# Kernel optimization log

Measured on AMD Instinct MI355X. Metric: run time of the kernel, lower is better.

## Reference

```python
import jax, jax.numpy as jnp
import numpy as np

L, B, S, H, NH, F = 4, 2, 1024, 1024, 16, 4096
DH = H // NH

def setup_inputs() -> dict:
    key = jax.random.key(0)
    ks = jax.random.split(key, 16)
    std = 0.02
    return {
        'x': jax.random.normal(ks[0], (B, S, H), jnp.float32),
        'attention_mask': jnp.ones((B, S, S), jnp.float32),
        'wq': jax.random.normal(ks[1], (L, H, H), jnp.float32) * std,
        'bq': jnp.zeros((L, H), jnp.float32),
        'wk': jax.random.normal(ks[2], (L, H, H), jnp.float32) * std,
        'bk': jnp.zeros((L, H), jnp.float32),
        'wv': jax.random.normal(ks[3], (L, H, H), jnp.float32) * std,
        'bv': jnp.zeros((L, H), jnp.float32),
        'wo_attn': jax.random.normal(ks[4], (L, H, H), jnp.float32) * std,
        'bo_attn': jnp.zeros((L, H), jnp.float32),
        'alpha_attn': jax.random.uniform(ks[5], (L,), jnp.float32) * 0.1,
        'wi': jax.random.normal(ks[6], (L, H, F), jnp.float32) * std,
        'bi': jnp.zeros((L, F), jnp.float32),
        'wo_ffn': jax.random.normal(ks[7], (L, F, H), jnp.float32) * std,
        'bo_ffn': jnp.zeros((L, H), jnp.float32),
        'alpha_ffn': jax.random.uniform(ks[8], (L,), jnp.float32) * 0.1,
    }

def _heads(t):
    # [B,S,H] -> [B,NH,S,DH]
    return t.reshape(B, S, NH, DH).transpose(0, 2, 1, 3)

def reference(x, attention_mask, wq, bq, wk, bk, wv, bv, wo_attn, bo_attn,
              alpha_attn, wi, bi, wo_ffn, bo_ffn, alpha_ffn):
    # additive mask: (1 - mask) * -10000, broadcast over heads
    adder = (1.0 - attention_mask)[:, None, :, :] * -10000.0  # [B,1,S,S]
    scale = 1.0 / jnp.sqrt(jnp.asarray(DH, x.dtype))
    for l in range(L):
        q = _heads(x @ wq[l] + bq[l])
        k = _heads(x @ wk[l] + bk[l])
        v = _heads(x @ wv[l] + bv[l])
        scores = jnp.einsum('bhqd,bhkd->bhqk', q, k) * scale + adder
        probs = jax.nn.softmax(scores, axis=-1)
        ctx = jnp.einsum('bhqk,bhkd->bhqd', probs, v)
        ctx = ctx.transpose(0, 2, 1, 3).reshape(B, S, H)
        attn_out = ctx @ wo_attn[l] + bo_attn[l]
        x = x + alpha_attn[l] * attn_out  # rezero residual
        inter = jax.nn.gelu(x @ wi[l] + bi[l], approximate=True)
        ffn_out = inter @ wo_ffn[l] + bo_ffn[l]
        x = x + alpha_ffn[l] * ffn_out  # rezero residual
    return x
```

## Files before the change

kernel.cpp:

```cpp
#include <hip/hip_runtime.h>
#include <cstdint>

#define B_  2
#define S_  1024
#define H_  1024
#define NH_ 16
#define DH_ 64
#define F_  4096
#define L_  4
#define M_  (B_*S_)

typedef __bf16 bf16;
typedef __bf16 bf16x8 __attribute__((ext_vector_type(8)));
typedef __bf16 bf16x4 __attribute__((ext_vector_type(4)));
typedef __bf16 bf16x2 __attribute__((ext_vector_type(2)));
typedef float  f32x4  __attribute__((ext_vector_type(4)));

__device__ __forceinline__ void async_ld16(void* lds, const void* g) {
  auto* lp = reinterpret_cast<__attribute__((address_space(3))) unsigned int*>(
      reinterpret_cast<uintptr_t>(lds));
  const auto* gp = reinterpret_cast<const __attribute__((address_space(1))) unsigned int*>(
      reinterpret_cast<uintptr_t>(g));
  __builtin_amdgcn_global_load_lds(gp, lp, 16, 0, 0);
}

__device__ __forceinline__ float gelu_tanh(float x) {
  float u = 0.7978845608028654f * (x + 0.044715f * x * x * x);
  u = fminf(fmaxf(u, -15.f), 15.f);
  float e = __builtin_amdgcn_exp2f(u * 2.8853900817779268f);
  return 0.5f * x * (1.f + (e - 1.f) / (e + 1.f));
}

__global__ __launch_bounds__(256) void transpose_all(
    const float* __restrict__ wq, const float* __restrict__ wk,
    const float* __restrict__ wv, const float* __restrict__ wo,
    const float* __restrict__ wi, const float* __restrict__ wf,
    bf16* __restrict__ WtQKV, bf16* __restrict__ WtO,
    bf16* __restrict__ WtI, bf16* __restrict__ WtF) {
  const size_t HH = (size_t)H_ * H_;
  const size_t HF = (size_t)H_ * F_;
  int idx = blockIdx.x;
  const float* src;
  bf16* dst;
  int N, K, k0, n0;
  if (idx < 4096) {
    const int s = idx >> 10;
    const int l = (idx >> 8) & 3;
    const int t = idx & 255;
    n0 = (t & 15) * 64; k0 = (t >> 4) * 64;
    N = H_; K = H_;
    src = (s == 0 ? wq : s == 1 ? wk : s == 2 ? wv : wo) + (size_t)l * HH;
    dst = (s < 3) ? (WtQKV + (size_t)l * 3 * HH + (size_t)s * HH)
                  : (WtO + (size_t)l * HH);
  } else if (idx < 8192) {
    const int j = idx - 4096;
    const int l = j >> 10;
    const int t = j & 1023;
    n0 = (t & 63) * 64; k0 = (t >> 6) * 64;
    N = F_; K = H_;
    src = wi + (size_t)l * HF;
    dst = WtI + (size_t)l * HF;
  } else {
    const int j = idx - 8192;
    const int l = j >> 10;
    const int t = j & 1023;
    n0 = (t & 15) * 64; k0 = (t >> 4) * 64;
    N = H_; K = F_;
    src = wf + (size_t)l * HF;
    dst = WtF + (size_t)l * HF;
  }
  __shared__ float t[64][65];
  const int x = threadIdx.x, y = threadIdx.y;
  #pragma unroll
  for (int i = 0; i < 64; i += 8) {
    const float2 v = *(const float2*)(src + (size_t)(k0 + y + i) * N + n0 + 2 * x);
    t[2 * x][y + i] = v.x;
    t[2 * x + 1][y + i] = v.y;
  }
  __syncthreads();
  #pragma unroll
  for (int i = 0; i < 64; i += 8) {
    bf16x2 o;
    o[0] = (bf16)t[y + i][2 * x];
    o[1] = (bf16)t[y + i][2 * x + 1];
    *(bf16x2*)(dst + (size_t)(n0 + y + i) * K + k0 + 2 * x) = o;
  }
}

__global__ __launch_bounds__(256) void prep_kernel(
    const float4* __restrict__ mask, bf16x4* __restrict__ madd,
    const float4* __restrict__ x, float4* __restrict__ xf,
    bf16x4* __restrict__ xb) {
  const int blk = blockIdx.x;
  if (blk < 2048) {
    const int i = blk * 256 + (int)threadIdx.x;
    const float c2 = -10000.f * 1.44269504088896f;
    float4 v = mask[i];
    bf16x4 o;
    o[0] = (bf16)((1.f - v.x) * c2);
    o[1] = (bf16)((1.f - v.y) * c2);
    o[2] = (bf16)((1.f - v.z) * c2);
    o[3] = (bf16)((1.f - v.w) * c2);
    madd[i] = o;
  } else {
    const int i = (blk - 2048) * 256 + (int)threadIdx.x;
    float4 v = x[i];
    xf[i] = v;
    bf16x4 b;
    b[0] = (bf16)v.x; b[1] = (bf16)v.y; b[2] = (bf16)v.z; b[3] = (bf16)v.w;
    xb[i] = b;
  }
}

__device__ __forceinline__ void gemm_core(
    const bf16* __restrict__ A, const bf16* __restrict__ Bt, int ld, int kLen,
    int m0, int n0, bf16* As, bf16* Bs, f32x4 (&acc)[4][4]) {
  const int tid = (int)threadIdx.x;
  const int w = tid >> 6, l = tid & 63;
  const int lr = l & 15, lg = l >> 4;
  const int wm = w >> 1, wn = w & 1;
  const int srow = l >> 2;
  const int scol = (l & 3) * 8;

  const bf16* ag = A  + (size_t)(m0 + w * 32 + srow) * ld + scol;
  const bf16* bg = Bt + (size_t)(n0 + w * 32 + srow) * ld + scol;
  const int soff = (w * 32) * 32;

  auto stage = [&](int buf, int kk) {
    bf16* ad = As + buf * 4096 + soff;
    bf16* bd = Bs + buf * 4096 + soff;
    async_ld16(ad,           ag + kk);
    async_ld16(ad + 16 * 32, ag + kk + (size_t)16 * ld);
    async_ld16(bd,           bg + kk);
    async_ld16(bd + 16 * 32, bg + kk + (size_t)16 * ld);
  };

  stage(0, 0);
  __syncthreads();
  int cur = 0;
  for (int k0 = 0; k0 < kLen; k0 += 32) {
    if (k0 + 32 < kLen) stage(cur ^ 1, k0 + 32);
    const bf16* Ab = As + cur * 4096;
    const bf16* Bb = Bs + cur * 4096;
    bf16x8 af[4], bv[4];
    #pragma unroll
    for (int i = 0; i < 4; ++i)
      af[i] = *(const bf16x8*)(Ab + (wm * 64 + i * 16 + lr) * 32 + lg * 8);
    #pragma unroll
    for (int i = 0; i < 4; ++i)
      bv[i] = *(const bf16x8*)(Bb + (wn * 64 + i * 16 + lr) * 32 + lg * 8);
    #pragma unroll
    for (int i = 0; i < 4; ++i)
      #pragma unroll
      for (int j = 0; j < 4; ++j)
        acc[i][j] = __builtin_amdgcn_mfma_f32_16x16x32_bf16(af[i], bv[j], acc[i][j], 0, 0, 0);
    __syncthreads();
    cur ^= 1;
  }
}

template <int MODE>
__global__ __launch_bounds__(256) void gemm128_kernel(
    const bf16* __restrict__ A, const bf16* __restrict__ Bt,
    const float* __restrict__ bias, bf16* __restrict__ outb,
    int N, int K, int kSlice) {
  __shared__ __align__(16) bf16 As[2 * 128 * 32];
  __shared__ __align__(16) bf16 Bs[2 * 128 * 32];
  const int m0 = blockIdx.y * 128, n0 = blockIdx.x * 128;
  const int z = blockIdx.z;
  const f32x4 z4 = {0.f, 0.f, 0.f, 0.f};
  f32x4 acc[4][4];
  #pragma unroll
  for (int i = 0; i < 4; ++i)
    #pragma unroll
    for (int j = 0; j < 4; ++j) acc[i][j] = z4;

  gemm_core(A + (size_t)z * kSlice, Bt + (size_t)z * kSlice, K, kSlice,
            m0, n0, As, Bs, acc);

  const int tid = (int)threadIdx.x;
  const int w = tid >> 6, l = tid & 63;
  const int lr = l & 15, lg = l >> 4;
  const int wm = w >> 1, wn = w & 1;
  const size_t pbase = (MODE == 3) ? (size_t)z * M_ * (size_t)N : 0;
  #pragma unroll
  for (int i = 0; i < 4; ++i) {
    const int row0 = m0 + wm * 64 + i * 16 + lg * 4;
    #pragma unroll
    for (int j = 0; j < 4; ++j) {
      const int col = n0 + wn * 64 + j * 16 + lr;
      const float bvx = (MODE == 3) ? 0.f : bias[col];
      #pragma unroll
      for (int r = 0; r < 4; ++r) {
        const size_t idx = (size_t)(row0 + r) * N + col;
        float v = acc[i][j][r] + bvx;
        if (MODE == 3) {
          outb[pbase + idx] = (bf16)v;
        } else {
          outb[idx] = (bf16)gelu_tanh(v);
        }
      }
    }
  }
}

__global__ __launch_bounds__(256) void reduce_residual(
    const bf16x4* __restrict__ part, const float* __restrict__ bias,
    const float* __restrict__ alphap, float4* __restrict__ xf,
    bf16x4* __restrict__ xb) {
  const int i = blockIdx.x * 256 + (int)threadIdx.x;
  const int nper = M_ * H_ / 4;
  float s[4] = {0.f, 0.f, 0.f, 0.f};
  #pragma unroll
  for (int zz = 0; zz < 4; ++zz) {
    const bf16x4 p = part[i + (size_t)zz * nper];
    #pragma unroll
    for (int k = 0; k < 4; ++k) s[k] += (float)p[k];
  }
  const int col = (i * 4) & (H_ - 1);
  const float4 b4 = *(const float4*)(bias + col);
  const float a = *alphap;
  float4 xv = xf[i];
  xv.x += a * (s[0] + b4.x);
  xv.y += a * (s[1] + b4.y);
  xv.z += a * (s[2] + b4.z);
  xv.w += a * (s[3] + b4.w);
  xf[i] = xv;
  bf16x4 bb;
  bb[0] = (bf16)xv.x; bb[1] = (bf16)xv.y; bb[2] = (bf16)xv.z; bb[3] = (bf16)xv.w;
  xb[i] = bb;
}

__global__ __launch_bounds__(256) void gemm_qkv64(
    const bf16* __restrict__ A, const bf16* __restrict__ Wt,
    const float* __restrict__ bq, const float* __restrict__ bk,
    const float* __restrict__ bvv,
    bf16* __restrict__ qo, bf16* __restrict__ ko, bf16* __restrict__ vt) {
  __shared__ __align__(16) bf16 As[2 * 128 * 32];
  __shared__ __align__(16) bf16 Bs[2 * 64 * 32];
  const int tid = (int)threadIdx.x;
  const int w = tid >> 6, l = tid & 63;
  const int lr = l & 15, lg = l >> 4;
  const int wm = w >> 1, wn = w & 1;
  const int srow = l >> 2, scol = (l & 3) * 8;
  const int m0 = blockIdx.y * 128, n0 = blockIdx.x * 64;

  const bf16* ag = A  + (size_t)(m0 + w * 32 + srow) * H_ + scol;
  const bf16* bg = Wt + (size_t)(n0 + w * 16 + srow) * H_ + scol;
  const int aoff = (w * 32) * 32;
  const int boff = (w * 16) * 32;

  auto stage = [&](int buf, int kk) {
    bf16* ad = As + buf * 4096 + aoff;
    bf16* bd = Bs + buf * 2048 + boff;
    async_ld16(ad,           ag + kk);
    async_ld16(ad + 16 * 32, ag + kk + (size_t)16 * H_);
    async_ld16(bd,           bg + kk);
  };

  const f32x4 z4 = {0.f, 0.f, 0.f, 0.f};
  f32x4 acc[4][2];
  #pragma unroll
  for (int i = 0; i < 4; ++i)
    #pragma unroll
    for (int j = 0; j < 2; ++j) acc[i][j] = z4;

  stage(0, 0);
  __syncthreads();
  int cur = 0;
  for (int k0 = 0; k0 < H_; k0 += 32) {
    if (k0 + 32 < H_) stage(cur ^ 1, k0 + 32);
    const bf16* Ab = As + cur * 4096;
    const bf16* Bb = Bs + cur * 2048;
    bf16x8 af[4], bv[2];
    #pragma unroll
    for (int i = 0; i < 4; ++i)
      af[i] = *(const bf16x8*)(Ab + (wm * 64 + i * 16 + lr) * 32 + lg * 8);
    #pragma unroll
    for (int j = 0; j < 2; ++j)
      bv[j] = *(const bf16x8*)(Bb + (wn * 32 + j * 16 + lr) * 32 + lg * 8);
    #pragma unroll
    for (int i = 0; i < 4; ++i)
      #pragma unroll
      for (int j = 0; j < 2; ++j)
        acc[i][j] = __builtin_amdgcn_mfma_f32_16x16x32_bf16(af[i], bv[j], acc[i][j], 0, 0, 0);
    __syncthreads();
    cur ^= 1;
  }

  if (n0 < 2048) {
    bf16* out = (n0 < 1024) ? qo : ko;
    const float* bias = (n0 < 1024) ? bq : bk;
    const int nl = n0 & 1023;
    #pragma unroll
    for (int i = 0; i < 4; ++i) {
      const int row0 = m0 + wm * 64 + i * 16 + lg * 4;
      #pragma unroll
      for (int j = 0; j < 2; ++j) {
        const int col = nl + wn * 32 + j * 16 + lr;
        const float bvx = bias[col];
        #pragma unroll
        for (int r = 0; r < 4; ++r)
          out[(size_t)(row0 + r) * H_ + col] = (bf16)(acc[i][j][r] + bvx);
      }
    }
  } else {
    const int hh = (n0 >> 6) - 32;
    #pragma unroll
    for (int i = 0; i < 4; ++i) {
      const int row0 = m0 + wm * 64 + i * 16 + lg * 4;
      const int bb = row0 >> 10, ss = row0 & (S_ - 1);
      #pragma unroll
      for (int j = 0; j < 2; ++j) {
        const int dd = wn * 32 + j * 16 + lr;
        const float bvx = bvv[hh * 64 + dd];
        bf16x4 pk;
        #pragma unroll
        for (int r = 0; r < 4; ++r) pk[r] = (bf16)(acc[i][j][r] + bvx);
        *(bf16x4*)(vt + (((size_t)(bb * NH_ + hh) * DH_ + dd) << 10) + ss) = pk;
      }
    }
  }
}

__global__ __launch_bounds__(256) void attn_kernel7(
    const bf16* __restrict__ Q, const bf16* __restrict__ Kb,
    const bf16* __restrict__ Vt, const bf16* __restrict__ madd,
    bf16* __restrict__ Ctx) {
  const int tid = (int)threadIdx.x;
  const int w = tid >> 6, l = tid & 63;
  const int lr = l & 15, lg = l >> 4;
  const int r7 = lr & 7;
  const int h = blockIdx.y, b = blockIdx.z;
  const int q0 = blockIdx.x * 64 + w * 16;

  __shared__ __align__(16) bf16 Kt[2][64 * 64];
  __shared__ __align__(16) bf16 Vs[2][64 * 64];
  __shared__ unsigned int Pu[4][16][36];

  const bf16* qp = Q + ((size_t)(b * S_ + q0 + lr)) * H_ + h * DH_;
  const bf16x8 qa0 = *(const bf16x8*)(qp + lg * 8);
  const bf16x8 qa1 = *(const bf16x8*)(qp + 32 + lg * 8);

  const f32x4 z4 = {0.f, 0.f, 0.f, 0.f};
  f32x4 acc[4];
  #pragma unroll
  for (int dt = 0; dt < 4; ++dt) acc[dt] = z4;
  float mrow = -1e30f, ssum = 0.f;

  const bf16* Kbase = Kb + ((size_t)b * S_) * H_ + h * DH_;
  const bf16* Vbase = Vt + ((size_t)(b * NH_ + h)) * DH_ * S_;
  const bf16* Mb = madd + ((size_t)(b * S_ + q0 + lr)) * S_;

  const float c1 = 0.125f * 1.44269504088896f;
  const float THR = 10.f;

  const int sub = l >> 3;
  const int cs  = ((l & 7) ^ sub) * 8;
  auto stage = [&](int buf, int kv) {
    #pragma unroll
    for (int j = 0; j < 2; ++j) {
      const int rbase = w * 16 + j * 8;
      async_ld16(&Kt[buf][rbase * 64],
                 Kbase + (size_t)(kv + rbase + sub) * H_ + cs);
      async_ld16(&Vs[buf][rbase * 64],
                 Vbase + (size_t)(rbase + sub) * S_ + kv + cs);
    }
  };

  stage(0, 0);
  bf16x4 mk[4];
  #pragma unroll
  for (int t = 0; t < 4; ++t) mk[t] = *(const bf16x4*)(Mb + t * 16 + lg * 4);
  __syncthreads();
  int cur = 0;
  #pragma unroll 1
  for (int it = 0; it < 16; ++it) {
    const int kv0 = it * 64;
    if (it < 15) stage(cur ^ 1, kv0 + 64);
    bf16x4 mkn[4];
    if (it < 15) {
      #pragma unroll
      for (int t = 0; t < 4; ++t)
        mkn[t] = *(const bf16x4*)(Mb + kv0 + 64 + t * 16 + lg * 4);
    }
    const bf16* Kc = &Kt[cur][0];
    const bf16* Vc = &Vs[cur][0];
    bf16x8 kf0[4], kf1[4];
    #pragma unroll
    for (int t = 0; t < 4; ++t) {
      kf0[t] = *(const bf16x8*)(Kc + (t * 16 + lr) * 64 + ((lg ^ r7) * 8));
      kf1[t] = *(const bf16x8*)(Kc + (t * 16 + lr) * 64 + (((4 + lg) ^ r7) * 8));
    }
    f32x4 st[4];
    __builtin_amdgcn_s_setprio(1);
    #pragma unroll
    for (int t = 0; t < 4; ++t) {
      f32x4 s = __builtin_amdgcn_mfma_f32_16x16x32_bf16(kf0[t], qa0, z4, 0, 0, 0);
      st[t] = __builtin_amdgcn_mfma_f32_16x16x32_bf16(kf1[t], qa1, s, 0, 0, 0);
    }
    __builtin_amdgcn_s_setprio(0);
    float sv[4][4];
    #pragma unroll
    for (int t = 0; t < 4; ++t)
      #pragma unroll
      for (int r = 0; r < 4; ++r)
        sv[t][r] = st[t][r] * c1 + (float)mk[t][r];
    float nm = sv[0][0];
    #pragma unroll
    for (int t = 0; t < 4; ++t)
      #pragma unroll
      for (int r = 0; r < 4; ++r) nm = fmaxf(nm, sv[t][r]);
    nm = fmaxf(nm, __shfl_xor(nm, 16));
    nm = fmaxf(nm, __shfl_xor(nm, 32));
    if (__any(nm > mrow + THR)) {
      float newm = fmaxf(mrow, nm);
      float f = __builtin_amdgcn_exp2f(mrow - newm);
      mrow = newm;
      ssum *= f;
      #pragma unroll
      for (int dt = 0; dt < 4; ++dt)
        #pragma unroll
        for (int r = 0; r < 4; ++r) acc[dt][r] *= f;
    }
    float p[4][4];
    float ps = 0.f;
    #pragma unroll
    for (int t = 0; t < 4; ++t)
      #pragma unroll
      for (int r = 0; r < 4; ++r) {
        p[t][r] = __builtin_amdgcn_exp2f(sv[t][r] - mrow);
        ps += p[t][r];
      }
    ps += __shfl_xor(ps, 16);
    ps += __shfl_xor(ps, 32);
    ssum += ps;
    #pragma unroll
    for (int t = 0; t < 4; ++t)
      #pragma unroll
      for (int hh = 0; hh < 2; ++hh) {
        union { bf16x2 v; unsigned int u; } pk;
        pk.v[0] = (bf16)p[t][2 * hh];
        pk.v[1] = (bf16)p[t][2 * hh + 1];
        Pu[w][lr][8 * t + 2 * lg + hh] = pk.u;
      }
    const bf16x8 pf0 = *(const bf16x8*)&Pu[w][lr][4 * lg];
    const bf16x8 pf1 = *(const bf16x8*)&Pu[w][lr][16 + 4 * lg];
    __builtin_amdgcn_s_setprio(1);
    #pragma unroll
    for (int dt = 0; dt < 4; ++dt) {
      bf16x8 vb0 = *(const bf16x8*)(Vc + (dt * 16 + lr) * 64 + ((lg ^ r7) * 8));
      acc[dt] = __builtin_amdgcn_mfma_f32_16x16x32_bf16(vb0, pf0, acc[dt], 0, 0, 0);
    }
    #pragma unroll
    for (int dt = 0; dt < 4; ++dt) {
      bf16x8 vb1 = *(const bf16x8*)(Vc + (dt * 16 + lr) * 64 + (((4 + lg) ^ r7) * 8));
      acc[dt] = __builtin_amdgcn_mfma_f32_16x16x32_bf16(vb1, pf1, acc[dt], 0, 0, 0);
    }
    __builtin_amdgcn_s_setprio(0);
    if (it < 15) {
      #pragma unroll
      for (int t = 0; t < 4; ++t) mk[t] = mkn[t];
    }
    __syncthreads();
    cur ^= 1;
  }
  const float inv = 1.f / ssum;
  bf16* cp = Ctx + ((size_t)(b * S_ + q0 + lr)) * H_ + h * DH_;
  #pragma unroll
  for (int dt = 0; dt < 4; ++dt) {
    bf16x4 o;
    #pragma unroll
    for (int r = 0; r < 4; ++r) o[r] = (bf16)(acc[dt][r] * inv);
    *(bf16x4*)(cp + dt * 16 + lg * 4) = o;
  }
}

extern "C" void kernel_launch(void* const* d_in, const int* in_sizes, int n_in,
                              void* d_out, int out_size, void* d_ws, size_t ws_size,
                              hipStream_t stream) {
  (void)in_sizes; (void)n_in; (void)out_size; (void)ws_size;
  const float* x    = (const float*)d_in[0];
  const float* mask = (const float*)d_in[1];
  const float* wq   = (const float*)d_in[2];
  const float* bq   = (const float*)d_in[3];
  const float* wk   = (const float*)d_in[4];
  const float* bk   = (const float*)d_in[5];
  const float* wv   = (const float*)d_in[6];
  const float* bv   = (const float*)d_in[7];
  const float* wo   = (const float*)d_in[8];
  const float* bo   = (const float*)d_in[9];
  const float* aat  = (const float*)d_in[10];
  const float* wi   = (const float*)d_in[11];
  const float* bi   = (const float*)d_in[12];
  const float* wf   = (const float*)d_in[13];
  const float* bf_  = (const float*)d_in[14];
  const float* afn  = (const float*)d_in[15];

  char* ws = (char*)d_ws;
  size_t o = 0;
  bf16* WtQKV = (bf16*)(ws + o); o += (size_t)L_ * 3 * H_ * H_ * 2;
  bf16* WtO = (bf16*)(ws + o); o += (size_t)L_ * H_ * H_ * 2;
  bf16* WtI = (bf16*)(ws + o); o += (size_t)L_ * H_ * F_ * 2;
  bf16* WtF = (bf16*)(ws + o); o += (size_t)L_ * F_ * H_ * 2;
  bf16* madd = (bf16*)(ws + o); o += (size_t)B_ * S_ * S_ * 2;
  bf16* xb  = (bf16*)(ws + o); o += (size_t)M_ * H_ * 2;
  bf16* qb  = (bf16*)(ws + o); o += (size_t)M_ * H_ * 2;
  bf16* kbf = (bf16*)(ws + o); o += (size_t)M_ * H_ * 2;
  bf16* vt  = (bf16*)(ws + o); o += (size_t)M_ * H_ * 2;
  bf16* ctx = (bf16*)(ws + o); o += (size_t)M_ * H_ * 2;
  bf16* itm = (bf16*)(ws + o); o += (size_t)M_ * F_ * 2;
  bf16* partb = (bf16*)(ws + o); o += (size_t)4 * M_ * H_ * 2;

  float* xf = (float*)d_out;

  const size_t HH = (size_t)H_ * H_;
  transpose_all<<<dim3(12288), dim3(32, 8), 0, stream>>>(
      wq, wk, wv, wo, wi, wf, WtQKV, WtO, WtI, WtF);
  prep_kernel<<<dim3(4096), 256, 0, stream>>>(
      (const float4*)mask, (bf16x4*)madd, (const float4*)x, (float4*)xf,
      (bf16x4*)xb);

  for (int l = 0; l < L_; ++l) {
    gemm_qkv64<<<dim3(48, M_/128), 256, 0, stream>>>(
        xb, WtQKV + (size_t)l * 3 * HH,
        bq + l * H_, bk + l * H_, bv + l * H_, qb, kbf, vt);
    attn_kernel7<<<dim3(S_/64, NH_, B_), 256, 0, stream>>>(
        qb, kbf, vt, madd, ctx);
    gemm128_kernel<3><<<dim3(H_/128, M_/128, 4), 256, 0, stream>>>(
        ctx, WtO + (size_t)l * HH, nullptr, partb, H_, H_, H_ / 4);
    reduce_residual<<<dim3((M_ * H_ / 4) / 256), 256, 0, stream>>>(
        (const bf16x4*)partb, bo + l * H_, aat + l, (float4*)xf, (bf16x4*)xb);
    gemm128_kernel<1><<<dim3(F_/128, M_/128), 256, 0, stream>>>(
        xb, WtI + (size_t)l * H_ * F_, bi + l * F_, itm, F_, H_, H_);
    gemm128_kernel<3><<<dim3(H_/128, M_/128, 4), 256, 0, stream>>>(
        itm, WtF + (size_t)l * F_ * H_, nullptr, partb, H_, F_, F_ / 4);
    reduce_residual<<<dim3((M_ * H_ / 4) / 256), 256, 0, stream>>>(
        (const bf16x4*)partb, bf_ + l * H_, afn + l, (float4*)xf, (bf16x4*)xb);
  }
}
```

Before: 606.5 us.

## Fuse weight transpose and bf16 cast into GEMM B-tile loading

Drops the upfront transpose_all kernel that converted every fp32 weight to transposed bf16. Each GEMM now reads fp32 weight rows straight from global memory into registers, casts them to bf16 and writes them transposed into a padded LDS tile, with the write placed after the MFMAs to overlap the loads. This avoids one pass over all weights, but every GEMM block now re-reads fp32 weights (twice the bytes of bf16) through register-staged loads instead of async LDS loads. It also adds VGPR pressure and possible LDS bank conflicts.

```diff
diff --git a/kernel.cpp b/kernel.cpp
--- a/kernel.cpp
+++ b/kernel.cpp
@@ -29,62 +29,6 @@
   u = fminf(fmaxf(u, -15.f), 15.f);
   float e = __builtin_amdgcn_exp2f(u * 2.8853900817779268f);
   return 0.5f * x * (1.f + (e - 1.f) / (e + 1.f));
-}
-
-__global__ __launch_bounds__(256) void transpose_all(
-    const float* __restrict__ wq, const float* __restrict__ wk,
-    const float* __restrict__ wv, const float* __restrict__ wo,
-    const float* __restrict__ wi, const float* __restrict__ wf,
-    bf16* __restrict__ WtQKV, bf16* __restrict__ WtO,
-    bf16* __restrict__ WtI, bf16* __restrict__ WtF) {
-  const size_t HH = (size_t)H_ * H_;
-  const size_t HF = (size_t)H_ * F_;
-  int idx = blockIdx.x;
-  const float* src;
-  bf16* dst;
-  int N, K, k0, n0;
-  if (idx < 4096) {
-    const int s = idx >> 10;
-    const int l = (idx >> 8) & 3;
-    const int t = idx & 255;
-    n0 = (t & 15) * 64; k0 = (t >> 4) * 64;
-    N = H_; K = H_;
-    src = (s == 0 ? wq : s == 1 ? wk : s == 2 ? wv : wo) + (size_t)l * HH;
-    dst = (s < 3) ? (WtQKV + (size_t)l * 3 * HH + (size_t)s * HH)
-                  : (WtO + (size_t)l * HH);
-  } else if (idx < 8192) {
-    const int j = idx - 4096;
-    const int l = j >> 10;
-    const int t = j & 1023;
-    n0 = (t & 63) * 64; k0 = (t >> 6) * 64;
-    N = F_; K = H_;
-    src = wi + (size_t)l * HF;
-    dst = WtI + (size_t)l * HF;
-  } else {
-    const int j = idx - 8192;
-    const int l = j >> 10;
-    const int t = j & 1023;
-    n0 = (t & 15) * 64; k0 = (t >> 4) * 64;
-    N = H_; K = F_;
-    src = wf + (size_t)l * HF;
-    dst = WtF + (size_t)l * HF;
-  }
-  __shared__ float t[64][65];
-  const int x = threadIdx.x, y = threadIdx.y;
-  #pragma unroll
-  for (int i = 0; i < 64; i += 8) {
-    const float2 v = *(const float2*)(src + (size_t)(k0 + y + i) * N + n0 + 2 * x);
-    t[2 * x][y + i] = v.x;
-    t[2 * x + 1][y + i] = v.y;
-  }
-  __syncthreads();
-  #pragma unroll
-  for (int i = 0; i < 64; i += 8) {
-    bf16x2 o;
-    o[0] = (bf16)t[y + i][2 * x];
-    o[1] = (bf16)t[y + i][2 * x + 1];
-    *(bf16x2*)(dst + (size_t)(n0 + y + i) * K + k0 + 2 * x) = o;
-  }
 }
 
 __global__ __launch_bounds__(256) void prep_kernel(
@@ -113,8 +57,8 @@
 }
 
 __device__ __forceinline__ void gemm_core(
-    const bf16* __restrict__ A, const bf16* __restrict__ Bt, int ld, int kLen,
-    int m0, int n0, bf16* As, bf16* Bs, f32x4 (&acc)[4][4]) {
+    const bf16* __restrict__ A, const float* __restrict__ W, int ldA, int N,
+    int kLen, int m0, int n0, bf16* As, bf16* Bs, f32x4 (&acc)[4][4]) {
   const int tid = (int)threadIdx.x;
   const int w = tid >> 6, l = tid & 63;
   const int lr = l & 15, lg = l >> 4;
@@ -122,38 +66,53 @@
   const int srow = l >> 2;
   const int scol = (l & 3) * 8;
 
-  const bf16* ag = A  + (size_t)(m0 + w * 32 + srow) * ld + scol;
-  const bf16* bg = Bt + (size_t)(n0 + w * 32 + srow) * ld + scol;
-  const int soff = (w * 32) * 32;
-
-  auto stage = [&](int buf, int kk) {
-    bf16* ad = As + buf * 4096 + soff;
-    bf16* bd = Bs + buf * 4096 + soff;
+  const bf16* ag = A + (size_t)(m0 + w * 32 + srow) * ldA + scol;
+  const int aoff = (w * 32) * 32;
+  const float* wg = W + (size_t)(w * 8) * N + n0 + 2 * l;
+
+  auto stageA = [&](int buf, int kk) {
+    bf16* ad = As + buf * 4096 + aoff;
     async_ld16(ad,           ag + kk);
-    async_ld16(ad + 16 * 32, ag + kk + (size_t)16 * ld);
-    async_ld16(bd,           bg + kk);
-    async_ld16(bd + 16 * 32, bg + kk + (size_t)16 * ld);
-  };
-
-  stage(0, 0);
+    async_ld16(ad + 16 * 32, ag + kk + (size_t)16 * ldA);
+  };
+  float2 bl[8];
+  auto loadB = [&](int kk) {
+    const float* p = wg + (size_t)kk * N;
+    #pragma unroll
+    for (int i = 0; i < 8; ++i) bl[i] = *(const float2*)(p + (size_t)i * N);
+  };
+  auto writeB = [&](int buf) {
+    bf16x8 v0, v1;
+    #pragma unroll
+    for (int i = 0; i < 8; ++i) { v0[i] = (bf16)bl[i].x; v1[i] = (bf16)bl[i].y; }
+    bf16* bd = Bs + buf * 5120;
+    *(bf16x8*)(bd + (2 * l) * 40 + w * 8)     = v0;
+    *(bf16x8*)(bd + (2 * l + 1) * 40 + w * 8) = v1;
+  };
+
+  stageA(0, 0);
+  loadB(0);
+  writeB(0);
   __syncthreads();
   int cur = 0;
   for (int k0 = 0; k0 < kLen; k0 += 32) {
-    if (k0 + 32 < kLen) stage(cur ^ 1, k0 + 32);
+    const bool more = (k0 + 32 < kLen);
+    if (more) { stageA(cur ^ 1, k0 + 32); loadB(k0 + 32); }
     const bf16* Ab = As + cur * 4096;
-    const bf16* Bb = Bs + cur * 4096;
+    const bf16* Bb = Bs + cur * 5120;
     bf16x8 af[4], bv[4];
     #pragma unroll
     for (int i = 0; i < 4; ++i)
       af[i] = *(const bf16x8*)(Ab + (wm * 64 + i * 16 + lr) * 32 + lg * 8);
     #pragma unroll
     for (int i = 0; i < 4; ++i)
-      bv[i] = *(const bf16x8*)(Bb + (wn * 64 + i * 16 + lr) * 32 + lg * 8);
+      bv[i] = *(const bf16x8*)(Bb + (wn * 64 + i * 16 + lr) * 40 + lg * 8);
     #pragma unroll
     for (int i = 0; i < 4; ++i)
       #pragma unroll
       for (int j = 0; j < 4; ++j)
         acc[i][j] = __builtin_amdgcn_mfma_f32_16x16x32_bf16(af[i], bv[j], acc[i][j], 0, 0, 0);
+    if (more) writeB(cur ^ 1);
     __syncthreads();
     cur ^= 1;
   }
@@ -161,11 +120,11 @@
 
 template <int MODE>
 __global__ __launch_bounds__(256) void gemm128_kernel(
-    const bf16* __restrict__ A, const bf16* __restrict__ Bt,
+    const bf16* __restrict__ A, const float* __restrict__ W,
     const float* __restrict__ bias, bf16* __restrict__ outb,
     int N, int K, int kSlice) {
   __shared__ __align__(16) bf16 As[2 * 128 * 32];
-  __shared__ __align__(16) bf16 Bs[2 * 128 * 32];
+  __shared__ __align__(16) bf16 Bs[2 * 128 * 40];
   const int m0 = blockIdx.y * 128, n0 = blockIdx.x * 128;
   const int z = blockIdx.z;
   const f32x4 z4 = {0.f, 0.f, 0.f, 0.f};
@@ -175,7 +134,7 @@
     #pragma unroll
     for (int j = 0; j < 4; ++j) acc[i][j] = z4;
 
-  gemm_core(A + (size_t)z * kSlice, Bt + (size_t)z * kSlice, K, kSlice,
+  gemm_core(A + (size_t)z * kSlice, W + (size_t)z * kSlice * N, K, N, kSlice,
             m0, n0, As, Bs, acc);
 
   const int tid = (int)threadIdx.x;
@@ -232,12 +191,13 @@
 }
 
 __global__ __launch_bounds__(256) void gemm_qkv64(
-    const bf16* __restrict__ A, const bf16* __restrict__ Wt,
+    const bf16* __restrict__ A, const float* __restrict__ wq,
+    const float* __restrict__ wk, const float* __restrict__ wv,
     const float* __restrict__ bq, const float* __restrict__ bk,
     const float* __restrict__ bvv,
     bf16* __restrict__ qo, bf16* __restrict__ ko, bf16* __restrict__ vt) {
   __shared__ __align__(16) bf16 As[2 * 128 * 32];
-  __shared__ __align__(16) bf16 Bs[2 * 64 * 32];
+  __shared__ __align__(16) bf16 Bs[2 * 64 * 40];
   const int tid = (int)threadIdx.x;
   const int w = tid >> 6, l = tid & 63;
   const int lr = l & 15, lg = l >> 4;
@@ -245,17 +205,29 @@
   const int srow = l >> 2, scol = (l & 3) * 8;
   const int m0 = blockIdx.y * 128, n0 = blockIdx.x * 64;
 
-  const bf16* ag = A  + (size_t)(m0 + w * 32 + srow) * H_ + scol;
-  const bf16* bg = Wt + (size_t)(n0 + w * 16 + srow) * H_ + scol;
+  const float* Wsel = (n0 < 1024) ? wq : (n0 < 2048) ? wk : wv;
+  const int nl = n0 & 1023;
+
+  const bf16* ag = A + (size_t)(m0 + w * 32 + srow) * H_ + scol;
   const int aoff = (w * 32) * 32;
-  const int boff = (w * 16) * 32;
-
-  auto stage = [&](int buf, int kk) {
+  const float* wg = Wsel + (size_t)(w * 8) * H_ + nl + l;
+
+  auto stageA = [&](int buf, int kk) {
     bf16* ad = As + buf * 4096 + aoff;
-    bf16* bd = Bs + buf * 2048 + boff;
     async_ld16(ad,           ag + kk);
     async_ld16(ad + 16 * 32, ag + kk + (size_t)16 * H_);
-    async_ld16(bd,           bg + kk);
+  };
+  float bl[8];
+  auto loadB = [&](int kk) {
+    const float* p = wg + (size_t)kk * H_;
+    #pragma unroll
+    for (int i = 0; i < 8; ++i) bl[i] = p[(size_t)i * H_];
+  };
+  auto writeB = [&](int buf) {
+    bf16x8 v0;
+    #pragma unroll
+    for (int i = 0; i < 8; ++i) v0[i] = (bf16)bl[i];
+    *(bf16x8*)(Bs + buf * 2560 + l * 40 + w * 8) = v0;
   };
 
   const f32x4 z4 = {0.f, 0.f, 0.f, 0.f};
@@ -265,25 +237,29 @@
     #pragma unroll
     for (int j = 0; j < 2; ++j) acc[i][j] = z4;
 
-  stage(0, 0);
+  stageA(0, 0);
+  loadB(0);
+  writeB(0);
   __syncthreads();
   int cur = 0;
   for (int k0 = 0; k0 < H_; k0 += 32) {
-    if (k0 + 32 < H_) stage(cur ^ 1, k0 + 32);
+    const bool more = (k0 + 32 < H_);
+    if (more) { stageA(cur ^ 1, k0 + 32); loadB(k0 + 32); }
     const bf16* Ab = As + cur * 4096;
-    const bf16* Bb = Bs + cur * 2048;
+    const bf16* Bb = Bs + cur * 2560;
     bf16x8 af[4], bv[2];
     #pragma unroll
     for (int i = 0; i < 4; ++i)
       af[i] = *(const bf16x8*)(Ab + (wm * 64 + i * 16 + lr) * 32 + lg * 8);
     #pragma unroll
     for (int j = 0; j < 2; ++j)
-      bv[j] = *(const bf16x8*)(Bb + (wn * 32 + j * 16 + lr) * 32 + lg * 8);
+      bv[j] = *(const bf16x8*)(Bb + (wn * 32 + j * 16 + lr) * 40 + lg * 8);
     #pragma unroll
     for (int i = 0; i < 4; ++i)
       #pragma unroll
       for (int j = 0; j < 2; ++j)
         acc[i][j] = __builtin_amdgcn_mfma_f32_16x16x32_bf16(af[i], bv[j], acc[i][j], 0, 0, 0);
+    if (more) writeB(cur ^ 1);
     __syncthreads();
     cur ^= 1;
   }
@@ -291,7 +267,6 @@
   if (n0 < 2048) {
     bf16* out = (n0 < 1024) ? qo : ko;
     const float* bias = (n0 < 1024) ? bq : bk;
-    const int nl = n0 & 1023;
     #pragma unroll
     for (int i = 0; i < 4; ++i) {
       const int row0 = m0 + wm * 64 + i * 16 + lg * 4;
@@ -499,10 +474,6 @@
 
   char* ws = (char*)d_ws;
   size_t o = 0;
-  bf16* WtQKV = (bf16*)(ws + o); o += (size_t)L_ * 3 * H_ * H_ * 2;
-  bf16* WtO = (bf16*)(ws + o); o += (size_t)L_ * H_ * H_ * 2;
-  bf16* WtI = (bf16*)(ws + o); o += (size_t)L_ * H_ * F_ * 2;
-  bf16* WtF = (bf16*)(ws + o); o += (size_t)L_ * F_ * H_ * 2;
   bf16* madd = (bf16*)(ws + o); o += (size_t)B_ * S_ * S_ * 2;
   bf16* xb  = (bf16*)(ws + o); o += (size_t)M_ * H_ * 2;
   bf16* qb  = (bf16*)(ws + o); o += (size_t)M_ * H_ * 2;
@@ -515,26 +486,25 @@
   float* xf = (float*)d_out;
 
   const size_t HH = (size_t)H_ * H_;
-  transpose_all<<<dim3(12288), dim3(32, 8), 0, stream>>>(
-      wq, wk, wv, wo, wi, wf, WtQKV, WtO, WtI, WtF);
+  const size_t HF = (size_t)H_ * F_;
   prep_kernel<<<dim3(4096), 256, 0, stream>>>(
       (const float4*)mask, (bf16x4*)madd, (const float4*)x, (float4*)xf,
       (bf16x4*)xb);
 
   for (int l = 0; l < L_; ++l) {
     gemm_qkv64<<<dim3(48, M_/128), 256, 0, stream>>>(
-        xb, WtQKV + (size_t)l * 3 * HH,
+        xb, wq + (size_t)l * HH, wk + (size_t)l * HH, wv + (size_t)l * HH,
         bq + l * H_, bk + l * H_, bv + l * H_, qb, kbf, vt);
     attn_kernel7<<<dim3(S_/64, NH_, B_), 256, 0, stream>>>(
         qb, kbf, vt, madd, ctx);
     gemm128_kernel<3><<<dim3(H_/128, M_/128, 4), 256, 0, stream>>>(
-        ctx, WtO + (size_t)l * HH, nullptr, partb, H_, H_, H_ / 4);
+        ctx, wo + (size_t)l * HH, nullptr, partb, H_, H_, H_ / 4);
     reduce_residual<<<dim3((M_ * H_ / 4) / 256), 256, 0, stream>>>(
         (const bf16x4*)partb, bo + l * H_, aat + l, (float4*)xf, (bf16x4*)xb);
     gemm128_kernel<1><<<dim3(F_/128, M_/128), 256, 0, stream>>>(
-        xb, WtI + (size_t)l * H_ * F_, bi + l * F_, itm, F_, H_, H_);
+        xb, wi + (size_t)l * HF, bi + l * F_, itm, F_, H_, H_);
     gemm128_kernel<3><<<dim3(H_/128, M_/128, 4), 256, 0, stream>>>(
-        itm, WtF + (size_t)l * F_ * H_, nullptr, partb, H_, F_, F_ / 4);
+        itm, wf + (size_t)l * HF, nullptr, partb, H_, F_, F_ / 4);
     reduce_residual<<<dim3((M_ * H_ / 4) / 256), 256, 0, stream>>>(
         (const bf16x4*)partb, bf_ + l * H_, afn + l, (float4*)xf, (bf16x4*)xb);
   }
```

Result: slower. 666.7 us (+9.9%).
